# Kernel optimization log

Measured on AMD Instinct MI355X. Metric: run time of the kernel, lower is better.

## Reference

```python
import jax, jax.numpy as jnp
import numpy as np

EPS_BN = 1e-5
NEG_SLOPE = 0.2

def gat_layer(x, src, dst, N, W, a_src, a_dst, b, heads, ch, concat):
    # x: [N, Fin]; W: [Fin, heads*ch]; a_src/a_dst: [heads, ch]; b: [heads*ch] or [ch]
    xw = (x @ W).reshape(N, heads, ch)                      # [N,H,C]
    al_src = jnp.einsum('nhc,hc->nh', xw, a_src)            # [N,H]
    al_dst = jnp.einsum('nhc,hc->nh', xw, a_dst)
    e = jax.nn.leaky_relu(al_src[src] + al_dst[dst], NEG_SLOPE)  # [E,H]
    m = jax.ops.segment_max(e, dst, num_segments=N)         # segment softmax (stable)
    ee = jnp.exp(e - m[dst])
    s = jax.ops.segment_sum(ee, dst, num_segments=N)
    alpha = ee / (s[dst] + 1e-16)                            # [E,H]
    msg = xw[src] * alpha[:, :, None]                        # [E,H,C]
    out = jax.ops.segment_sum(msg, dst, num_segments=N)      # [N,H,C]
    if concat:
        return out.reshape(N, heads * ch) + b
    return out.mean(axis=1) + b

def setup_inputs():
    key = jax.random.key(0)
    ks = jax.random.split(key, 24)
    N, E, dim_in, dim_out = 20000, 320000, 256, 16
    x = jax.random.normal(ks[0], (N, dim_in), dtype=jnp.float32)
    edge_index = jax.random.randint(ks[1], (2, E), 0, N, dtype=jnp.int64)
    def glorot(k, shape):
        fan = shape[0] + shape[-1]
        return jax.random.uniform(k, shape, jnp.float32, -1.0, 1.0) * np.sqrt(6.0 / fan)
    return {
        'x': x, 'edge_index': edge_index,
        'bn_gamma': jnp.ones((dim_in,), jnp.float32),
        'bn_beta': jnp.zeros((dim_in,), jnp.float32),
        'W1': glorot(ks[2], (dim_in, 16 * 64)),
        'a1_src': glorot(ks[3], (16, 64)), 'a1_dst': glorot(ks[4], (16, 64)),
        'b1': jnp.zeros((16 * 64,), jnp.float32),
        'p1': jnp.float32(0.25),
        'W2': glorot(ks[5], (dim_in + 16 * 64, 8 * 8)),
        'a2_src': glorot(ks[6], (8, 8)), 'a2_dst': glorot(ks[7], (8, 8)),
        'b2': jnp.zeros((8 * 8,), jnp.float32),
        'p2': jnp.float32(0.25),
        'W3': glorot(ks[8], (8 * 8, 8 * dim_out)),
        'a3_src': glorot(ks[9], (8, dim_out)), 'a3_dst': glorot(ks[10], (8, dim_out)),
        'b3': jnp.zeros((dim_out,), jnp.float32),
    }

def reference(x, edge_index, bn_gamma, bn_beta, W1, a1_src, a1_dst, b1, p1,
              W2, a2_src, a2_dst, b2, p2, W3, a3_src, a3_dst, b3):
    N = x.shape[0]
    # PyG GATConv default add_self_loops=True
    loops = jnp.arange(N, dtype=edge_index.dtype)
    src = jnp.concatenate([edge_index[0], loops])
    dst = jnp.concatenate([edge_index[1], loops])
    # BatchNorm1d (training-mode batch stats)
    mu = x.mean(axis=0)
    var = x.var(axis=0)
    x_in = (x - mu) * jax.lax.rsqrt(var + EPS_BN) * bn_gamma + bn_beta
    h = gat_layer(x_in, src, dst, N, W1, a1_src, a1_dst, b1, 16, 64, True)
    h = jnp.where(h >= 0, h, p1 * h)  # PReLU
    h = gat_layer(jnp.concatenate([x_in, h], axis=1), src, dst, N, W2, a2_src, a2_dst, b2, 8, 8, True)
    h = jnp.where(h >= 0, h, p2 * h)
    h = gat_layer(h, src, dst, N, W3, a3_src, a3_dst, b3, 8, b3.shape[0], False)
    return jax.nn.log_softmax(h, axis=1)
```

## Files before the change

### kernel.cpp

```cpp
#include <hip/hip_runtime.h>
#include <math.h>

typedef unsigned int u32;
typedef unsigned short u16;
typedef u32 u32x4 __attribute__((ext_vector_type(4)));
typedef float f32x4 __attribute__((ext_vector_type(4)));

__device__ __forceinline__ u16 f2bf(float f) {
  u32 u = __builtin_bit_cast(u32, f);
  return (u16)((u + 0x7FFFu + ((u >> 16) & 1u)) >> 16);
}
__device__ __forceinline__ float bf2f(u32 lo16) {
  return __builtin_bit_cast(float, lo16 << 16);
}
__device__ __forceinline__ void mfma16(f32x4& c, const u32x4& a, const u32x4& b) {
  asm volatile("v_mfma_f32_16x16x32_bf16 %0, %1, %2, %0" : "+v"(c) : "v"(a), "v"(b));
}
__device__ __forceinline__ float lrelu(float e) { return fmaxf(e, 0.2f * e); }

__global__ void bn_stats_kernel(const float* __restrict__ x, float* __restrict__ musum,
                                float* __restrict__ sqsum, int N, int F) {
  int t = threadIdx.x;
  float s = 0.f, s2 = 0.f;
  for (int r = blockIdx.x; r < N; r += gridDim.x) {
    float v = x[(size_t)r * F + t];
    s += v;
    s2 += v * v;
  }
  atomicAdd(&musum[t], s);
  atomicAdd(&sqsum[t], s2);
}

__global__ void bn_finalize_kernel(const float* __restrict__ musum, const float* __restrict__ sqsum,
                                   const float* __restrict__ gamma, const float* __restrict__ beta,
                                   float* __restrict__ scale, float* __restrict__ shift, int N) {
  int t = threadIdx.x;
  float m = musum[t] / (float)N;
  float v = sqsum[t] / (float)N - m * m;
  float sc = gamma[t] * rsqrtf(v + 1e-5f);
  scale[t] = sc;
  shift[t] = beta[t] - m * sc;
}

__global__ void bn_apply_bf16_kernel(const float* __restrict__ x, const float* __restrict__ scale,
                                     const float* __restrict__ shift, u16* __restrict__ xin,
                                     int total, int Fmask) {
  int i = blockIdx.x * blockDim.x + threadIdx.x;
  if (i < total) {
    int c = i & Fmask;
    xin[i] = f2bf(x[i] * scale[c] + shift[c]);
  }
}

__global__ void csr_count_kernel(const int* __restrict__ ei, int E, int N, int* __restrict__ cnt) {
  int e = blockIdx.x * blockDim.x + threadIdx.x;
  int ET = E + N;
  if (e < ET) {
    int d = (e < E) ? ei[E + e] : (e - E);
    atomicAdd(&cnt[d], 1);
  }
}

__global__ void csr_scan_kernel(const int* __restrict__ cnt, int* __restrict__ row_ptr,
                                int* __restrict__ cursor, int N) {
  __shared__ int part[256];
  int t = threadIdx.x;
  int chunk = (N + 255) / 256;
  int lo = t * chunk;
  int hi = min(lo + chunk, N);
  int s = 0;
  for (int i = lo; i < hi; i++) s += cnt[i];
  part[t] = s;
  __syncthreads();
  for (int off = 1; off < 256; off <<= 1) {
    int v = (t >= off) ? part[t - off] : 0;
    __syncthreads();
    part[t] += v;
    __syncthreads();
  }
  int run = (t == 0) ? 0 : part[t - 1];
  for (int i = lo; i < hi; i++) {
    row_ptr[i] = run;
    cursor[i] = run;
    run += cnt[i];
  }
  if (t == 255) row_ptr[N] = part[255];
}

__global__ void csr_fill_kernel(const int* __restrict__ ei, int E, int N,
                                int* __restrict__ cursor, int* __restrict__ csr_src) {
  int e = blockIdx.x * blockDim.x + threadIdx.x;
  int ET = E + N;
  if (e < ET) {
    int s, d;
    if (e < E) { s = ei[e]; d = ei[E + e]; }
    else       { s = e - E; d = s; }
    int pos = atomicAdd(&cursor[d], 1);
    csr_src[pos] = s;
  }
}

__global__ void wt_build_all(const float* __restrict__ W1, const float* __restrict__ W2,
                             const float* __restrict__ W3, u16* __restrict__ Wt1,
                             u16* __restrict__ Wt2, u16* __restrict__ Wt3) {
  const int S1 = 256 * 1024, S2 = 1280 * 64, S3 = 64 * 128;
  int idx = blockIdx.x * blockDim.x + threadIdx.x;
  if (idx < S1) {
    int n = idx / 256, k = idx % 256;
    Wt1[idx] = f2bf(W1[(size_t)k * 1024 + n]);
  } else if (idx < S1 + S2) {
    int i = idx - S1;
    int n = i / 1280, k = i % 1280;
    Wt2[i] = f2bf(W2[(size_t)k * 64 + n]);
  } else if (idx < S1 + S2 + S3) {
    int i = idx - S1 - S2;
    int n = i / 64, k = i % 64;
    Wt3[i] = f2bf(W3[(size_t)k * 128 + n]);
  }
}

__global__ void alfold_build(const float* __restrict__ W1, const float* __restrict__ a1s,
                             const float* __restrict__ a1d, const float* __restrict__ W2,
                             const float* __restrict__ a2s, const float* __restrict__ a2d,
                             const float* __restrict__ W3, const float* __restrict__ a3s,
                             const float* __restrict__ a3d, u16* __restrict__ alf1,
                             u16* __restrict__ alf2, u16* __restrict__ alf3) {
  const int T1 = 32 * 256, T2 = 32 * 1280, T3 = 32 * 64;
  int idx = blockIdx.x * blockDim.x + threadIdx.x;
  if (idx < T1) {
    int jj = idx / 256, k = idx % 256, h = jj >> 1;
    const float* av = (jj & 1) ? a1d : a1s;
    float s = 0.f;
    for (int c = 0; c < 64; c++) s += W1[(size_t)k * 1024 + h * 64 + c] * av[h * 64 + c];
    alf1[idx] = f2bf(s);
  } else if (idx < T1 + T2) {
    int i = idx - T1;
    int jj = i / 1280, k = i % 1280, h = jj >> 1;
    float s = 0.f;
    if (h < 8) {
      const float* av = (jj & 1) ? a2d : a2s;
      for (int c = 0; c < 8; c++) s += W2[(size_t)k * 64 + h * 8 + c] * av[h * 8 + c];
    }
    alf2[i] = f2bf(s);
  } else if (idx < T1 + T2 + T3) {
    int i = idx - T1 - T2;
    int jj = i / 64, k = i % 64, h = jj >> 1;
    float s = 0.f;
    if (h < 8) {
      const float* av = (jj & 1) ? a3d : a3s;
      for (int c = 0; c < 16; c++) s += W3[(size_t)k * 128 + h * 16 + c] * av[h * 16 + c];
    }
    alf3[i] = f2bf(s);
  }
}

template <int BM, int BN, int FM, int FN>
__global__ __launch_bounds__(256) void mfma_gemm_kernel(
    const u16* __restrict__ A1, const u16* __restrict__ A2, int K1, int K,
    const u16* __restrict__ Wt, u16* __restrict__ Ch, int M, int Nc) {
  constexpr int BK = 32;
  constexpr int CA = (BM * BK) / (256 * 8);
  constexpr int CB = (BN * BK) / (256 * 8);
  static_assert(BM == 2 * FM * 16 && BN == 2 * FN * 16, "wave grid 2x2");
  __shared__ u16 As[BM * BK];
  __shared__ u16 Bs[BN * BK];
  int t = threadIdx.x;
  int m0 = blockIdx.x * BM, n0 = blockIdx.y * BN;
  int r = t & 15;
  int g = (t >> 4) & 3;
  int wid = t >> 6;
  int wm0 = (wid >> 1) * (FM * 16);
  int wn0 = (wid & 1) * (FN * 16);
  int K8 = K >> 3;
  int K2 = K - K1;

  f32x4 acc[FM][FN] = {};
  asm volatile("s_nop 7\n\ts_nop 7" :::);

  for (int k0 = 0; k0 < K; k0 += BK) {
    const u16* Aseg;
    int sA, kl;
    if (k0 < K1) { Aseg = A1; sA = K1; kl = k0; }
    else         { Aseg = A2; sA = K2; kl = k0 - K1; }
    __syncthreads();
#pragma unroll
    for (int i = 0; i < CA; i++) {
      int c = i * 256 + t;
      int m = c >> 2, kb = c & 3;
      *(u32x4*)(As + c * 8) =
          *(const u32x4*)(Aseg + (size_t)(m0 + m) * sA + kl + kb * 8);
    }
#pragma unroll
    for (int i = 0; i < CB; i++) {
      int c = i * 256 + t;
      int nn = c >> 2, kb = c & 3;
      *(u32x4*)(Bs + c * 8) =
          *(const u32x4*)(Wt + ((size_t)(n0 + nn) * K8 + (k0 >> 3) + kb) * 8);
    }
    __syncthreads();
    u32x4 af[FM], bfr[FN];
#pragma unroll
    for (int fi = 0; fi < FM; fi++)
      af[fi] = *(const u32x4*)(As + ((wm0 + fi * 16 + r) * 4 + g) * 8);
#pragma unroll
    for (int fj = 0; fj < FN; fj++)
      bfr[fj] = *(const u32x4*)(Bs + ((wn0 + fj * 16 + r) * 4 + g) * 8);
#pragma unroll
    for (int fi = 0; fi < FM; fi++)
#pragma unroll
      for (int fj = 0; fj < FN; fj++) mfma16(acc[fi][fj], af[fi], bfr[fj]);
  }
  asm volatile("s_nop 7\n\ts_nop 7" :::);

#pragma unroll
  for (int fi = 0; fi < FM; fi++) {
#pragma unroll
    for (int fj = 0; fj < FN; fj++) {
#pragma unroll
      for (int v = 0; v < 4; v++) {
        int m = m0 + wm0 + fi * 16 + g * 4 + v;
        int nn = n0 + wn0 + fj * 16 + r;
        if (m < M) Ch[(size_t)m * Nc + nn] = f2bf(acc[fi][fj][v]);
      }
    }
  }
}

template <int FM, int H>
__global__ __launch_bounds__(256) void al_gemm_kernel(
    const u16* __restrict__ A1, const u16* __restrict__ A2, int K1, int K,
    const u16* __restrict__ alf, float* __restrict__ als, float* __restrict__ ald, int M) {
  constexpr int BM = 2 * FM * 16, BN = 32, BK = 32;
  constexpr int CA = (BM * BK) / (256 * 8);
  __shared__ u16 As[BM * BK];
  __shared__ u16 Bs[BN * BK];
  int t = threadIdx.x;
  int m0 = blockIdx.x * BM;
  int r = t & 15, g = (t >> 4) & 3, wid = t >> 6;
  int wm0 = (wid >> 1) * (FM * 16);
  int wn0 = (wid & 1) * 16;
  int K8 = K >> 3, K2 = K - K1;
  f32x4 acc[FM] = {};
  asm volatile("s_nop 7\n\ts_nop 7" :::);
  for (int k0 = 0; k0 < K; k0 += BK) {
    const u16* Aseg;
    int sA, kl;
    if (k0 < K1) { Aseg = A1; sA = K1; kl = k0; }
    else         { Aseg = A2; sA = K2; kl = k0 - K1; }
    __syncthreads();
#pragma unroll
    for (int i = 0; i < CA; i++) {
      int c = i * 256 + t;
      int mm = c >> 2, kb = c & 3;
      *(u32x4*)(As + c * 8) =
          *(const u32x4*)(Aseg + (size_t)(m0 + mm) * sA + kl + kb * 8);
    }
    if (t < (BN * BK) / 8) {
      int nn = t >> 2, kb = t & 3;
      *(u32x4*)(Bs + t * 8) = *(const u32x4*)(alf + ((size_t)nn * K8 + (k0 >> 3) + kb) * 8);
    }
    __syncthreads();
    u32x4 bfr = *(const u32x4*)(Bs + ((wn0 + r) * 4 + g) * 8);
#pragma unroll
    for (int fi = 0; fi < FM; fi++) {
      u32x4 af = *(const u32x4*)(As + ((wm0 + fi * 16 + r) * 4 + g) * 8);
      mfma16(acc[fi], af, bfr);
    }
  }
  asm volatile("s_nop 7\n\ts_nop 7" :::);
  int nn = wn0 + r;
  if (nn < 2 * H) {
    float* dst = (nn & 1) ? ald : als;
    int hh = nn >> 1;
#pragma unroll
    for (int fi = 0; fi < FM; fi++) {
#pragma unroll
      for (int v = 0; v < 4; v++) {
        int mm = m0 + wm0 + fi * 16 + g * 4 + v;
        if (mm < M) dst[(size_t)mm * H + hh] = acc[fi][v];
      }
    }
  }
}

__global__ __launch_bounds__(256) void gat_agg1_wave(
    const u16* __restrict__ xwh, const float* __restrict__ alsrc,
    const float* __restrict__ aldst, const int* __restrict__ row_ptr,
    const int* __restrict__ csr_src, const float* __restrict__ bias,
    const float* __restrict__ slope_p, u16* __restrict__ out, int N) {
  constexpr int U = 6;
  int wid = blockIdx.x * 4 + (threadIdx.x >> 6);
  int n = wid >> 1, q = wid & 1;
  if (n >= N) return;
  int lane = threadIdx.x & 63;
  int head = q * 8 + (lane >> 3), g = lane & 7;
  float ad = aldst[(size_t)n * 16 + head];
  int start = row_ptr[n];
  int end = row_ptr[n + 1];
  int deg = end - start;
  int endm1 = end - 1;

  float m = -1e30f, s = 0.f;
  for (int j = g; j < deg; j += 8) {
    int sj = csr_src[start + j];
    float e = lrelu(alsrc[(size_t)sj * 16 + head] + ad);
    float mn = fmaxf(m, e);
    s = s * __expf(m - mn) + __expf(e - mn);
    m = mn;
  }
#pragma unroll
  for (int st = 1; st <= 4; st <<= 1) {
    float m2 = __shfl_xor(m, st);
    float s2 = __shfl_xor(s, st);
    float mn = fmaxf(m, m2);
    s = s * __expf(m - mn) + s2 * __expf(m2 - mn);
    m = mn;
  }
  float rr = 1.f / (s + 1e-16f);

  float acc[8] = {};
  const u16* base = xwh + (size_t)q * 512 + (size_t)lane * 8;

  auto fma8 = [&](const u32x4& v, float w) {
#pragma unroll
    for (int i = 0; i < 4; i++) {
      u32 u = v[i];
      acc[2 * i] = fmaf(w, bf2f(u & 0xffffu), acc[2 * i]);
      acc[2 * i + 1] = fmaf(w, bf2f(u >> 16), acc[2 * i + 1]);
    }
  };

  int c[U];
#pragma unroll
  for (int i = 0; i < U; i++) c[i] = csr_src[min(start + i, endm1)];
  int j = 0;
  for (; j + U <= deg; j += U) {
    u32x4 v[U];
    float a[U];
#pragma unroll
    for (int i = 0; i < U; i++) v[i] = *(const u32x4*)(base + (size_t)c[i] * 1024);
#pragma unroll
    for (int i = 0; i < U; i++) a[i] = alsrc[(size_t)c[i] * 16 + head];
#pragma unroll
    for (int i = 0; i < U; i++) c[i] = csr_src[min(start + j + U + i, endm1)];
#pragma unroll
    for (int i = 0; i < U; i++) {
      float w = __expf(lrelu(a[i] + ad) - m) * rr;
      fma8(v[i], w);
    }
  }
  for (int i = 0; j < deg; j++, i++) {
    u32x4 v = *(const u32x4*)(base + (size_t)c[i] * 1024);
    float a = alsrc[(size_t)c[i] * 16 + head];
    float w = __expf(lrelu(a + ad) - m) * rr;
    fma8(v, w);
  }

  float p = slope_p[0];
  u32 ow[4];
#pragma unroll
  for (int i = 0; i < 4; i++) {
    int cc = q * 512 + lane * 8 + 2 * i;
    float v0 = acc[2 * i] + bias[cc];
    float v1 = acc[2 * i + 1] + bias[cc + 1];
    v0 = (v0 >= 0.f) ? v0 : p * v0;
    v1 = (v1 >= 0.f) ? v1 : p * v1;
    ow[i] = (u32)f2bf(v0) | ((u32)f2bf(v1) << 16);
  }
  *(u32x4*)((u32*)(out + (size_t)n * 1024 + q * 512) + lane * 4) = *(u32x4*)ow;
}

__global__ __launch_bounds__(256) void gat_agg2_wave(
    const u16* __restrict__ xwh, const float* __restrict__ alsrc,
    const float* __restrict__ aldst, const int* __restrict__ row_ptr,
    const int* __restrict__ csr_src, const float* __restrict__ bias,
    const float* __restrict__ slope_p, u16* __restrict__ out, int N) {
  constexpr int U = 8;
  int n = blockIdx.x * 4 + (threadIdx.x >> 6);
  if (n >= N) return;
  int lane = threadIdx.x & 63;
  int head = lane >> 3, g = lane & 7;
  float ad = aldst[(size_t)n * 8 + head];
  int start = row_ptr[n];
  int end = row_ptr[n + 1];
  int deg = end - start;
  int endm1 = end - 1;

  float m = -1e30f, s = 0.f;
  for (int j = g; j < deg; j += 8) {
    int sj = csr_src[start + j];
    float e = lrelu(alsrc[(size_t)sj * 8 + head] + ad);
    float mn = fmaxf(m, e);
    s = s * __expf(m - mn) + __expf(e - mn);
    m = mn;
  }
#pragma unroll
  for (int st = 1; st <= 4; st <<= 1) {
    float m2 = __shfl_xor(m, st);
    float s2 = __shfl_xor(s, st);
    float mn = fmaxf(m, m2);
    s = s * __expf(m - mn) + s2 * __expf(m2 - mn);
    m = mn;
  }
  float rr = 1.f / (s + 1e-16f);

  float acc = 0.f;
  int c[U];
#pragma unroll
  for (int i = 0; i < U; i++) c[i] = csr_src[min(start + i, endm1)];
  int j = 0;
  for (; j + U <= deg; j += U) {
    u16 v[U];
    float a[U];
#pragma unroll
    for (int i = 0; i < U; i++) v[i] = xwh[(size_t)c[i] * 64 + lane];
#pragma unroll
    for (int i = 0; i < U; i++) a[i] = alsrc[(size_t)c[i] * 8 + head];
#pragma unroll
    for (int i = 0; i < U; i++) c[i] = csr_src[min(start + j + U + i, endm1)];
#pragma unroll
    for (int i = 0; i < U; i++) {
      float w = __expf(lrelu(a[i] + ad) - m) * rr;
      acc = fmaf(w, bf2f(v[i]), acc);
    }
  }
  for (int i = 0; j < deg; j++, i++) {
    float v = bf2f(xwh[(size_t)c[i] * 64 + lane]);
    float w = __expf(lrelu(alsrc[(size_t)c[i] * 8 + head] + ad) - m) * rr;
    acc = fmaf(w, v, acc);
  }

  float p = slope_p[0];
  float v = acc + bias[lane];
  out[(size_t)n * 64 + lane] = f2bf((v >= 0.f) ? v : p * v);
}

__global__ __launch_bounds__(256) void gat_agg3_wave(
    const u16* __restrict__ xwh, const float* __restrict__ alsrc,
    const float* __restrict__ aldst, const int* __restrict__ row_ptr,
    const int* __restrict__ csr_src, const float* __restrict__ bias,
    float* __restrict__ out, int N) {
  constexpr int U = 8;
  int n = blockIdx.x * 4 + (threadIdx.x >> 6);
  if (n >= N) return;
  int lane = threadIdx.x & 63;
  int head = lane >> 3, g = lane & 7;
  float ad = aldst[(size_t)n * 8 + head];
  int start = row_ptr[n];
  int end = row_ptr[n + 1];
  int deg = end - start;
  int endm1 = end - 1;

  float m = -1e30f, s = 0.f;
  for (int j = g; j < deg; j += 8) {
    int sj = csr_src[start + j];
    float e = lrelu(alsrc[(size_t)sj * 8 + head] + ad);
    float mn = fmaxf(m, e);
    s = s * __expf(m - mn) + __expf(e - mn);
    m = mn;
  }
#pragma unroll
  for (int st = 1; st <= 4; st <<= 1) {
    float m2 = __shfl_xor(m, st);
    float s2 = __shfl_xor(s, st);
    float mn = fmaxf(m, m2);
    s = s * __expf(m - mn) + s2 * __expf(m2 - mn);
    m = mn;
  }
  float rr = 1.f / (s + 1e-16f);

  float a0 = 0.f, a1 = 0.f;
  int c[U];
#pragma unroll
  for (int i = 0; i < U; i++) c[i] = csr_src[min(start + i, endm1)];
  int j = 0;
  for (; j + U <= deg; j += U) {
    u32 v[U];
    float a[U];
#pragma unroll
    for (int i = 0; i < U; i++) v[i] = *(const u32*)(xwh + (size_t)c[i] * 128 + lane * 2);
#pragma unroll
    for (int i = 0; i < U; i++) a[i] = alsrc[(size_t)c[i] * 8 + head];
#pragma unroll
    for (int i = 0; i < U; i++) c[i] = csr_src[min(start + j + U + i, endm1)];
#pragma unroll
    for (int i = 0; i < U; i++) {
      float w = __expf(lrelu(a[i] + ad) - m) * rr;
      a0 = fmaf(w, bf2f(v[i] & 0xffffu), a0);
      a1 = fmaf(w, bf2f(v[i] >> 16), a1);
    }
  }
  for (int i = 0; j < deg; j++, i++) {
    u32 v = *(const u32*)(xwh + (size_t)c[i] * 128 + lane * 2);
    float w = __expf(lrelu(alsrc[(size_t)c[i] * 8 + head] + ad) - m) * rr;
    a0 = fmaf(w, bf2f(v & 0xffffu), a0);
    a1 = fmaf(w, bf2f(v >> 16), a1);
  }

#pragma unroll
  for (int st = 8; st <= 32; st <<= 1) {
    a0 += __shfl_xor(a0, st);
    a1 += __shfl_xor(a1, st);
  }
  int c0 = (2 * lane) & 15, c1 = (2 * lane + 1) & 15;
  float v0 = a0 * 0.125f + bias[c0];
  float v1 = a1 * 0.125f + bias[c1];
  float mx = fmaxf(v0, v1);
#pragma unroll
  for (int st = 1; st <= 4; st <<= 1) mx = fmaxf(mx, __shfl_xor(mx, st));
  float se = __expf(v0 - mx) + __expf(v1 - mx);
#pragma unroll
  for (int st = 1; st <= 4; st <<= 1) se += __shfl_xor(se, st);
  float lse = mx + logf(se);
  if (lane < 8) {
    float2 o = make_float2(v0 - lse, v1 - lse);
    *((float2*)(out + (size_t)n * 16) + lane) = o;
  }
}

extern "C" void kernel_launch(void* const* d_in, const int* in_sizes, int n_in,
                              void* d_out, int out_size, void* d_ws, size_t ws_size,
                              hipStream_t stream) {
  const float* x        = (const float*)d_in[0];
  const int*   ei       = (const int*)d_in[1];
  const float* bn_gamma = (const float*)d_in[2];
  const float* bn_beta  = (const float*)d_in[3];
  const float* W1       = (const float*)d_in[4];
  const float* a1s      = (const float*)d_in[5];
  const float* a1d      = (const float*)d_in[6];
  const float* b1       = (const float*)d_in[7];
  const float* p1       = (const float*)d_in[8];
  const float* W2       = (const float*)d_in[9];
  const float* a2s      = (const float*)d_in[10];
  const float* a2d      = (const float*)d_in[11];
  const float* b2       = (const float*)d_in[12];
  const float* p2       = (const float*)d_in[13];
  const float* W3       = (const float*)d_in[14];
  const float* a3s      = (const float*)d_in[15];
  const float* a3d      = (const float*)d_in[16];
  const float* b3       = (const float*)d_in[17];
  float* out = (float*)d_out;

  const int F  = in_sizes[2];
  const int N  = in_sizes[0] / F;
  const int E  = in_sizes[1] / 2;
  const int ET = E + N;
  const int MP = ((N + 127) / 128) * 128;

  size_t off = 0;
  auto alloc = [&](size_t bytes) -> char* {
    char* r = (char*)d_ws + off;
    off += (bytes + 255) & ~(size_t)255;
    return r;
  };
  float* musum   = (float*)alloc(F * 4);
  float* sqsum   = (float*)alloc(F * 4);
  float* scale   = (float*)alloc(F * 4);
  float* shift   = (float*)alloc(F * 4);
  int*   row_ptr = (int*)alloc((size_t)(N + 1) * 4);
  int*   cursor  = (int*)alloc((size_t)N * 4);
  int*   csr_src = (int*)alloc((size_t)ET * 4);
  float* al_s    = (float*)alloc((size_t)N * 16 * 4);
  float* al_d    = (float*)alloc((size_t)N * 16 * 4);
  u16*   Wt1     = (u16*)alloc((size_t)256 * 1024 * 2);
  u16*   Wt2     = (u16*)alloc((size_t)1280 * 64 * 2);
  u16*   Wt3     = (u16*)alloc((size_t)64 * 128 * 2);
  u16*   alf1    = (u16*)alloc((size_t)32 * 256 * 2);
  u16*   alf2    = (u16*)alloc((size_t)32 * 1280 * 2);
  u16*   alf3    = (u16*)alloc((size_t)32 * 64 * 2);
  u16*   x_in_h  = (u16*)alloc((size_t)MP * 256 * 2);
  u16*   xw1h    = (u16*)alloc((size_t)MP * 1024 * 2);
  u16*   h1      = (u16*)alloc((size_t)MP * 1024 * 2);
  u16*   xw2h    = (u16*)alloc((size_t)MP * 64 * 2);
  u16*   h2h     = (u16*)alloc((size_t)MP * 64 * 2);
  u16*   xw3h    = (u16*)alloc((size_t)MP * 128 * 2);

  hipMemsetAsync(musum, 0, (size_t)2 * F * 4, stream);
  bn_stats_kernel<<<256, 256, 0, stream>>>(x, musum, sqsum, N, F);
  bn_finalize_kernel<<<1, F, 0, stream>>>(musum, sqsum, bn_gamma, bn_beta, scale, shift, N);
  int totalXF = N * F;
  bn_apply_bf16_kernel<<<(totalXF + 255) / 256, 256, 0, stream>>>(x, scale, shift, x_in_h,
                                                                  totalXF, F - 1);

  hipMemsetAsync(cursor, 0, (size_t)N * 4, stream);
  csr_count_kernel<<<(ET + 255) / 256, 256, 0, stream>>>(ei, E, N, cursor);
  csr_scan_kernel<<<1, 256, 0, stream>>>(cursor, row_ptr, cursor, N);
  csr_fill_kernel<<<(ET + 255) / 256, 256, 0, stream>>>(ei, E, N, cursor, csr_src);

  {
    int total = 256 * 1024 + 1280 * 64 + 64 * 128;
    wt_build_all<<<(total + 255) / 256, 256, 0, stream>>>(W1, W2, W3, Wt1, Wt2, Wt3);
    int tot2 = 32 * 256 + 32 * 1280 + 32 * 64;
    alfold_build<<<(tot2 + 255) / 256, 256, 0, stream>>>(W1, a1s, a1d, W2, a2s, a2d, W3, a3s, a3d,
                                                         alf1, alf2, alf3);
  }

  int nblk = (N + 3) / 4;

  {
    dim3 grid(MP / 128, 1024 / 128);
    mfma_gemm_kernel<128, 128, 4, 4><<<grid, 256, 0, stream>>>(
        x_in_h, x_in_h, 256, 256, Wt1, xw1h, N, 1024);
    al_gemm_kernel<4, 16><<<MP / 128, 256, 0, stream>>>(x_in_h, x_in_h, 256, 256, alf1, al_s, al_d,
                                                        N);
    gat_agg1_wave<<<(2 * N + 3) / 4, 256, 0, stream>>>(xw1h, al_s, al_d, row_ptr, csr_src, b1, p1,
                                                       h1, N);
  }

  {
    dim3 grid((N + 63) / 64, 1);
    mfma_gemm_kernel<64, 64, 2, 2><<<grid, 256, 0, stream>>>(
        x_in_h, h1, 256, 1280, Wt2, xw2h, N, 64);
    al_gemm_kernel<4, 8><<<MP / 128, 256, 0, stream>>>(x_in_h, h1, 256, 1280, alf2, al_s, al_d, N);
    gat_agg2_wave<<<nblk, 256, 0, stream>>>(xw2h, al_s, al_d, row_ptr, csr_src, b2, p2, h2h, N);
  }

  {
    dim3 grid((N + 63) / 64, 128 / 64);
    mfma_gemm_kernel<64, 64, 2, 2><<<grid, 256, 0, stream>>>(
        h2h, h2h, 64, 64, Wt3, xw3h, N, 128);
    al_gemm_kernel<4, 8><<<MP / 128, 256, 0, stream>>>(h2h, h2h, 64, 64, alf3, al_s, al_d, N);
    gat_agg3_wave<<<nblk, 256, 0, stream>>>(xw3h, al_s, al_d, row_ptr, csr_src, b3, out, N);
  }
}
```

Before: 368.4 us.

## Fuse attention-logit GEMM into feature GEMM by appending folded columns to weights

The folded attention vectors are appended as extra output columns of each layer's transposed weight matrix, so one MFMA GEMM produces both the projected features and the per-node source/destination logits. This removes the separate al_gemm launches and their second pass over the activation matrix. Layers 2 and 3 now use wider single-column-block tiles (96 and 160 columns), while layer 1 adds a ninth column block that is mostly zero padding. The CSR scan is also widened to 1024 threads.

```diff
diff --git a/kernel.cpp b/kernel.cpp
--- a/kernel.cpp
+++ b/kernel.cpp
@@ -61,18 +61,19 @@
   }
 }
 
-__global__ void csr_scan_kernel(const int* __restrict__ cnt, int* __restrict__ row_ptr,
-                                int* __restrict__ cursor, int N) {
-  __shared__ int part[256];
+__global__ __launch_bounds__(1024) void csr_scan_kernel(const int* __restrict__ cnt,
+                                                        int* __restrict__ row_ptr,
+                                                        int* __restrict__ cursor, int N) {
+  __shared__ int part[1024];
   int t = threadIdx.x;
-  int chunk = (N + 255) / 256;
+  int chunk = (N + 1023) / 1024;
   int lo = t * chunk;
   int hi = min(lo + chunk, N);
   int s = 0;
   for (int i = lo; i < hi; i++) s += cnt[i];
   part[t] = s;
   __syncthreads();
-  for (int off = 1; off < 256; off <<= 1) {
+  for (int off = 1; off < 1024; off <<= 1) {
     int v = (t >= off) ? part[t - off] : 0;
     __syncthreads();
     part[t] += v;
@@ -84,7 +85,7 @@
     cursor[i] = run;
     run += cnt[i];
   }
-  if (t == 255) row_ptr[N] = part[255];
+  if (t == 1023) row_ptr[N] = part[1023];
 }
 
 __global__ void csr_fill_kernel(const int* __restrict__ ei, int E, int N,
@@ -103,7 +104,8 @@
 __global__ void wt_build_all(const float* __restrict__ W1, const float* __restrict__ W2,
                              const float* __restrict__ W3, u16* __restrict__ Wt1,
                              u16* __restrict__ Wt2, u16* __restrict__ Wt3) {
-  const int S1 = 256 * 1024, S2 = 1280 * 64, S3 = 64 * 128;
+  const int S1 = 1024 * 256, S2 = 64 * 1280, S3 = 128 * 64;
+  const int P1 = 96 * 256, P2 = 32 * 1280, P3 = 32 * 64;
   int idx = blockIdx.x * blockDim.x + threadIdx.x;
   if (idx < S1) {
     int n = idx / 256, k = idx % 256;
@@ -116,6 +118,12 @@
     int i = idx - S1 - S2;
     int n = i / 64, k = i % 64;
     Wt3[i] = f2bf(W3[(size_t)k * 128 + n]);
+  } else if (idx < S1 + S2 + S3 + P1) {
+    Wt1[S1 + (idx - S1 - S2 - S3)] = 0;
+  } else if (idx < S1 + S2 + S3 + P1 + P2) {
+    Wt2[S2 + (idx - S1 - S2 - S3 - P1)] = 0;
+  } else if (idx < S1 + S2 + S3 + P1 + P2 + P3) {
+    Wt3[S3 + (idx - S1 - S2 - S3 - P1 - P2)] = 0;
   }
 }
 
@@ -123,44 +131,41 @@
                              const float* __restrict__ a1d, const float* __restrict__ W2,
                              const float* __restrict__ a2s, const float* __restrict__ a2d,
                              const float* __restrict__ W3, const float* __restrict__ a3s,
-                             const float* __restrict__ a3d, u16* __restrict__ alf1,
-                             u16* __restrict__ alf2, u16* __restrict__ alf3) {
-  const int T1 = 32 * 256, T2 = 32 * 1280, T3 = 32 * 64;
+                             const float* __restrict__ a3d, u16* __restrict__ Wt1,
+                             u16* __restrict__ Wt2, u16* __restrict__ Wt3) {
+  const int T1 = 32 * 256, T2 = 16 * 1280, T3 = 16 * 64;
   int idx = blockIdx.x * blockDim.x + threadIdx.x;
   if (idx < T1) {
     int jj = idx / 256, k = idx % 256, h = jj >> 1;
     const float* av = (jj & 1) ? a1d : a1s;
     float s = 0.f;
     for (int c = 0; c < 64; c++) s += W1[(size_t)k * 1024 + h * 64 + c] * av[h * 64 + c];
-    alf1[idx] = f2bf(s);
+    Wt1[(size_t)(1024 + jj) * 256 + k] = f2bf(s);
   } else if (idx < T1 + T2) {
     int i = idx - T1;
     int jj = i / 1280, k = i % 1280, h = jj >> 1;
+    const float* av = (jj & 1) ? a2d : a2s;
     float s = 0.f;
-    if (h < 8) {
-      const float* av = (jj & 1) ? a2d : a2s;
-      for (int c = 0; c < 8; c++) s += W2[(size_t)k * 64 + h * 8 + c] * av[h * 8 + c];
-    }
-    alf2[i] = f2bf(s);
+    for (int c = 0; c < 8; c++) s += W2[(size_t)k * 64 + h * 8 + c] * av[h * 8 + c];
+    Wt2[(size_t)(64 + jj) * 1280 + k] = f2bf(s);
   } else if (idx < T1 + T2 + T3) {
     int i = idx - T1 - T2;
     int jj = i / 64, k = i % 64, h = jj >> 1;
+    const float* av = (jj & 1) ? a3d : a3s;
     float s = 0.f;
-    if (h < 8) {
-      const float* av = (jj & 1) ? a3d : a3s;
-      for (int c = 0; c < 16; c++) s += W3[(size_t)k * 128 + h * 16 + c] * av[h * 16 + c];
-    }
-    alf3[i] = f2bf(s);
+    for (int c = 0; c < 16; c++) s += W3[(size_t)k * 128 + h * 16 + c] * av[h * 16 + c];
+    Wt3[(size_t)(128 + jj) * 64 + k] = f2bf(s);
   }
 }
 
 template <int BM, int BN, int FM, int FN>
-__global__ __launch_bounds__(256) void mfma_gemm_kernel(
+__global__ __launch_bounds__(256) void mfma_gemm_al(
     const u16* __restrict__ A1, const u16* __restrict__ A2, int K1, int K,
-    const u16* __restrict__ Wt, u16* __restrict__ Ch, int M, int Nc) {
+    const u16* __restrict__ Wt, u16* __restrict__ Ch, int NcH,
+    float* __restrict__ als, float* __restrict__ ald, int ALN, int M) {
   constexpr int BK = 32;
-  constexpr int CA = (BM * BK) / (256 * 8);
-  constexpr int CB = (BN * BK) / (256 * 8);
+  constexpr int ACH = (BM * BK) / 8;
+  constexpr int BCH = (BN * BK) / 8;
   static_assert(BM == 2 * FM * 16 && BN == 2 * FN * 16, "wave grid 2x2");
   __shared__ u16 As[BM * BK];
   __shared__ u16 Bs[BN * BK];
@@ -184,18 +189,22 @@
     else         { Aseg = A2; sA = K2; kl = k0 - K1; }
     __syncthreads();
 #pragma unroll
-    for (int i = 0; i < CA; i++) {
+    for (int i = 0; i < (ACH + 255) / 256; i++) {
       int c = i * 256 + t;
-      int m = c >> 2, kb = c & 3;
-      *(u32x4*)(As + c * 8) =
-          *(const u32x4*)(Aseg + (size_t)(m0 + m) * sA + kl + kb * 8);
-    }
-#pragma unroll
-    for (int i = 0; i < CB; i++) {
+      if (ACH % 256 == 0 || c < ACH) {
+        int m = c >> 2, kb = c & 3;
+        *(u32x4*)(As + c * 8) =
+            *(const u32x4*)(Aseg + (size_t)(m0 + m) * sA + kl + kb * 8);
+      }
+    }
+#pragma unroll
+    for (int i = 0; i < (BCH + 255) / 256; i++) {
       int c = i * 256 + t;
-      int nn = c >> 2, kb = c & 3;
-      *(u32x4*)(Bs + c * 8) =
-          *(const u32x4*)(Wt + ((size_t)(n0 + nn) * K8 + (k0 >> 3) + kb) * 8);
+      if (BCH % 256 == 0 || c < BCH) {
+        int nn = c >> 2, kb = c & 3;
+        *(u32x4*)(Bs + c * 8) =
+            *(const u32x4*)(Wt + ((size_t)(n0 + nn) * K8 + (k0 >> 3) + kb) * 8);
+      }
     }
     __syncthreads();
     u32x4 af[FM], bfr[FN];
@@ -220,64 +229,15 @@
       for (int v = 0; v < 4; v++) {
         int m = m0 + wm0 + fi * 16 + g * 4 + v;
         int nn = n0 + wn0 + fj * 16 + r;
-        if (m < M) Ch[(size_t)m * Nc + nn] = f2bf(acc[fi][fj][v]);
-      }
-    }
-  }
-}
-
-template <int FM, int H>
-__global__ __launch_bounds__(256) void al_gemm_kernel(
-    const u16* __restrict__ A1, const u16* __restrict__ A2, int K1, int K,
-    const u16* __restrict__ alf, float* __restrict__ als, float* __restrict__ ald, int M) {
-  constexpr int BM = 2 * FM * 16, BN = 32, BK = 32;
-  constexpr int CA = (BM * BK) / (256 * 8);
-  __shared__ u16 As[BM * BK];
-  __shared__ u16 Bs[BN * BK];
-  int t = threadIdx.x;
-  int m0 = blockIdx.x * BM;
-  int r = t & 15, g = (t >> 4) & 3, wid = t >> 6;
-  int wm0 = (wid >> 1) * (FM * 16);
-  int wn0 = (wid & 1) * 16;
-  int K8 = K >> 3, K2 = K - K1;
-  f32x4 acc[FM] = {};
-  asm volatile("s_nop 7\n\ts_nop 7" :::);
-  for (int k0 = 0; k0 < K; k0 += BK) {
-    const u16* Aseg;
-    int sA, kl;
-    if (k0 < K1) { Aseg = A1; sA = K1; kl = k0; }
-    else         { Aseg = A2; sA = K2; kl = k0 - K1; }
-    __syncthreads();
-#pragma unroll
-    for (int i = 0; i < CA; i++) {
-      int c = i * 256 + t;
-      int mm = c >> 2, kb = c & 3;
-      *(u32x4*)(As + c * 8) =
-          *(const u32x4*)(Aseg + (size_t)(m0 + mm) * sA + kl + kb * 8);
-    }
-    if (t < (BN * BK) / 8) {
-      int nn = t >> 2, kb = t & 3;
-      *(u32x4*)(Bs + t * 8) = *(const u32x4*)(alf + ((size_t)nn * K8 + (k0 >> 3) + kb) * 8);
-    }
-    __syncthreads();
-    u32x4 bfr = *(const u32x4*)(Bs + ((wn0 + r) * 4 + g) * 8);
-#pragma unroll
-    for (int fi = 0; fi < FM; fi++) {
-      u32x4 af = *(const u32x4*)(As + ((wm0 + fi * 16 + r) * 4 + g) * 8);
-      mfma16(acc[fi], af, bfr);
-    }
-  }
-  asm volatile("s_nop 7\n\ts_nop 7" :::);
-  int nn = wn0 + r;
-  if (nn < 2 * H) {
-    float* dst = (nn & 1) ? ald : als;
-    int hh = nn >> 1;
-#pragma unroll
-    for (int fi = 0; fi < FM; fi++) {
-#pragma unroll
-      for (int v = 0; v < 4; v++) {
-        int mm = m0 + wm0 + fi * 16 + g * 4 + v;
-        if (mm < M) dst[(size_t)mm * H + hh] = acc[fi][v];
+        if (m < M) {
+          float val = acc[fi][fj][v];
+          if (nn < NcH) {
+            Ch[(size_t)m * NcH + nn] = f2bf(val);
+          } else {
+            int j = nn - NcH;
+            if (j < ALN) ((j & 1) ? ald : als)[(size_t)m * (ALN >> 1) + (j >> 1)] = val;
+          }
+        }
       }
     }
   }
@@ -562,12 +522,9 @@
   int*   csr_src = (int*)alloc((size_t)ET * 4);
   float* al_s    = (float*)alloc((size_t)N * 16 * 4);
   float* al_d    = (float*)alloc((size_t)N * 16 * 4);
-  u16*   Wt1     = (u16*)alloc((size_t)256 * 1024 * 2);
-  u16*   Wt2     = (u16*)alloc((size_t)1280 * 64 * 2);
-  u16*   Wt3     = (u16*)alloc((size_t)64 * 128 * 2);
-  u16*   alf1    = (u16*)alloc((size_t)32 * 256 * 2);
-  u16*   alf2    = (u16*)alloc((size_t)32 * 1280 * 2);
-  u16*   alf3    = (u16*)alloc((size_t)32 * 64 * 2);
+  u16*   Wt1     = (u16*)alloc((size_t)1152 * 256 * 2);
+  u16*   Wt2     = (u16*)alloc((size_t)96 * 1280 * 2);
+  u16*   Wt3     = (u16*)alloc((size_t)160 * 64 * 2);
   u16*   x_in_h  = (u16*)alloc((size_t)MP * 256 * 2);
   u16*   xw1h    = (u16*)alloc((size_t)MP * 1024 * 2);
   u16*   h1      = (u16*)alloc((size_t)MP * 1024 * 2);
@@ -584,42 +541,38 @@
 
   hipMemsetAsync(cursor, 0, (size_t)N * 4, stream);
   csr_count_kernel<<<(ET + 255) / 256, 256, 0, stream>>>(ei, E, N, cursor);
-  csr_scan_kernel<<<1, 256, 0, stream>>>(cursor, row_ptr, cursor, N);
+  csr_scan_kernel<<<1, 1024, 0, stream>>>(cursor, row_ptr, cursor, N);
   csr_fill_kernel<<<(ET + 255) / 256, 256, 0, stream>>>(ei, E, N, cursor, csr_src);
 
   {
-    int total = 256 * 1024 + 1280 * 64 + 64 * 128;
+    int total = 1024 * 256 + 64 * 1280 + 128 * 64 + 96 * 256 + 32 * 1280 + 32 * 64;
     wt_build_all<<<(total + 255) / 256, 256, 0, stream>>>(W1, W2, W3, Wt1, Wt2, Wt3);
-    int tot2 = 32 * 256 + 32 * 1280 + 32 * 64;
+    int tot2 = 32 * 256 + 16 * 1280 + 16 * 64;
     alfold_build<<<(tot2 + 255) / 256, 256, 0, stream>>>(W1, a1s, a1d, W2, a2s, a2d, W3, a3s, a3d,
-                                                         alf1, alf2, alf3);
+                                                         Wt1, Wt2, Wt3);
   }
 
   int nblk = (N + 3) / 4;
 
   {
-    dim3 grid(MP / 128, 1024 / 128);
-    mfma_gemm_kernel<128, 128, 4, 4><<<grid, 256, 0, stream>>>(
-        x_in_h, x_in_h, 256, 256, Wt1, xw1h, N, 1024);
-    al_gemm_kernel<4, 16><<<MP / 128, 256, 0, stream>>>(x_in_h, x_in_h, 256, 256, alf1, al_s, al_d,
-                                                        N);
+    dim3 grid(MP / 128, 9);
+    mfma_gemm_al<128, 128, 4, 4><<<grid, 256, 0, stream>>>(
+        x_in_h, x_in_h, 256, 256, Wt1, xw1h, 1024, al_s, al_d, 32, N);
     gat_agg1_wave<<<(2 * N + 3) / 4, 256, 0, stream>>>(xw1h, al_s, al_d, row_ptr, csr_src, b1, p1,
                                                        h1, N);
   }
 
   {
     dim3 grid((N + 63) / 64, 1);
-    mfma_gemm_kernel<64, 64, 2, 2><<<grid, 256, 0, stream>>>(
-        x_in_h, h1, 256, 1280, Wt2, xw2h, N, 64);
-    al_gemm_kernel<4, 8><<<MP / 128, 256, 0, stream>>>(x_in_h, h1, 256, 1280, alf2, al_s, al_d, N);
+    mfma_gemm_al<64, 96, 2, 3><<<grid, 256, 0, stream>>>(
+        x_in_h, h1, 256, 1280, Wt2, xw2h, 64, al_s, al_d, 16, N);
     gat_agg2_wave<<<nblk, 256, 0, stream>>>(xw2h, al_s, al_d, row_ptr, csr_src, b2, p2, h2h, N);
   }
 
   {
-    dim3 grid((N + 63) / 64, 128 / 64);
-    mfma_gemm_kernel<64, 64, 2, 2><<<grid, 256, 0, stream>>>(
-        h2h, h2h, 64, 64, Wt3, xw3h, N, 128);
-    al_gemm_kernel<4, 8><<<MP / 128, 256, 0, stream>>>(h2h, h2h, 64, 64, alf3, al_s, al_d, N);
+    dim3 grid((N + 63) / 64, 1);
+    mfma_gemm_al<64, 160, 2, 5><<<grid, 256, 0, stream>>>(
+        h2h, h2h, 64, 64, Wt3, xw3h, 128, al_s, al_d, 16, N);
     gat_agg3_wave<<<nblk, 256, 0, stream>>>(xw3h, al_s, al_d, row_ptr, csr_src, b3, out, N);
   }
 }
```

After: 343.7 us. 6.7% less time.
